# Kernel tuning notes

Measured on AMD Instinct MI355X. Metric: run time of the kernel, lower is better.

The kernel has to match this reference:

```python
import jax, jax.numpy as jnp
import numpy as np

B, S, H, HK, D = 2, 2048, 32, 8, 128
R = 128            # rotary_dim
SINK = 128         # sink_len (always-visible prefix tokens in KV cache)
MAXPOS = 4096
BASE = 10000.0
SCALE = 0.08838834764831845  # 1/sqrt(head_size)
NEG = -1e30


def setup_inputs() -> dict:
    key = jax.random.key(0)
    ks = jax.random.split(key, 5)
    q = jax.random.normal(ks[0], (B, S, H, D), jnp.float32)
    k = jax.random.normal(ks[1], (B, S, HK, D), jnp.float32)
    v = jax.random.normal(ks[2], (B, S, HK, D), jnp.float32)
    sink_k = jax.random.normal(ks[3], (B, SINK, HK, D), jnp.float32)
    sink_v = jax.random.normal(ks[4], (B, SINK, HK, D), jnp.float32)
    # vLLM-style cache: row p = concat(cos(p*inv_freq), sin(p*inv_freq)), each R/2 wide
    inv_freq = 1.0 / (BASE ** (jnp.arange(0, R, 2, dtype=jnp.float32) / R))
    t = jnp.arange(MAXPOS, dtype=jnp.float32)
    freqs = jnp.outer(t, inv_freq)                      # [MAXPOS, R/2]
    cos_sin_cache = jnp.concatenate([jnp.cos(freqs), jnp.sin(freqs)], axis=-1)
    positions = jnp.arange(S, dtype=jnp.int32)
    return {"q": q, "k": k, "v": v, "sink_k": sink_k, "sink_v": sink_v,
            "cos_sin_cache": cos_sin_cache, "positions": positions}


def _apply_rope_neox(x, cos, sin):
    # x: [B, S, N, D]; cos/sin: [S, R/2]
    x_rot, x_pass = x[..., :R], x[..., R:]
    half = R // 2
    x1, x2 = x_rot[..., :half], x_rot[..., half:]
    c = cos[None, :, None, :]
    s = sin[None, :, None, :]
    o1 = x1 * c - x2 * s
    o2 = x2 * c + x1 * s
    return jnp.concatenate([o1, o2, x_pass], axis=-1)


def reference(q, k, v, sink_k, sink_v, cos_sin_cache, positions):
    # RoPE on q and k (sink KV already cached post-RoPE at their positions)
    cos_sin = cos_sin_cache[positions]                  # [S, R]
    cos, sin = cos_sin[:, :R // 2], cos_sin[:, R // 2:]
    q = _apply_rope_neox(q, cos, sin)
    k = _apply_rope_neox(k, cos, sin)

    # Prepend sink KV: effective kv length = SINK + S
    k_full = jnp.concatenate([sink_k, k], axis=1)       # [B, SINK+S, HK, D]
    v_full = jnp.concatenate([sink_v, v], axis=1)

    # GQA: expand kv heads to query heads
    rep = H // HK
    k_full = jnp.repeat(k_full, rep, axis=2)            # [B, SINK+S, H, D]
    v_full = jnp.repeat(v_full, rep, axis=2)

    scores = jnp.einsum('bqhd,bkhd->bhqk', q, k_full) * SCALE  # [B,H,S,SINK+S]

    # sink tokens always visible; causal over the real sequence
    q_idx = jnp.arange(S)[:, None]
    k_idx = jnp.arange(SINK + S)[None, :]
    mask = (k_idx < SINK) | ((k_idx - SINK) <= q_idx)   # [S, SINK+S]
    scores = jnp.where(mask[None, None], scores, NEG)

    attn = jax.nn.softmax(scores, axis=-1)
    out = jnp.einsum('bhqk,bkhd->bqhd', attn, v_full)   # [B,S,H,D]
    return out
```

## Files before the change

kernel.cpp:

```cpp
#include <hip/hip_runtime.h>

#define B_    2
#define S_    2048
#define H_    32
#define HK_   8
#define D_    128
#define SINK_ 128
#define KV_   (SINK_ + S_)
#define SCALE_L2E 0.12752139f

typedef unsigned short u16;
typedef unsigned int   u32;
typedef float  f32x4  __attribute__((ext_vector_type(4)));
typedef __bf16 bf16x8 __attribute__((ext_vector_type(8)));
typedef short  s16x8  __attribute__((ext_vector_type(8)));

__device__ __forceinline__ u16 f2bf(float f) {
    union { float f; u32 u; } c; c.f = f;
    u32 u = c.u;
    return (u16)((u + 0x7FFFu + ((u >> 16) & 1u)) >> 16);
}

#define PREPK_BLOCKS 8704
#define PREPV_BLOCKS 544

__global__ __launch_bounds__(256) void prep_kv(
    const float* __restrict__ k, const float* __restrict__ sk,
    const float* __restrict__ v, const float* __restrict__ sv,
    const float* __restrict__ csc, const int* __restrict__ pos,
    u16* __restrict__ kall,
    u16* __restrict__ vt)
{
    __shared__ u16 t[128][66];
    const int tid = threadIdx.x;
    if ((int)blockIdx.x < PREPK_BLOCKS) {
        int g  = blockIdx.x * 256 + tid;
        int i  = g & 63;
        int rw = g >> 6;
        int bh = rw / KV_;
        int j  = rw - bh * KV_;
        int hk = bh & (HK_ - 1);
        int b  = bh >> 3;
        float o1, o2;
        if (j < SINK_) {
            size_t src = ((size_t)(b * SINK_ + j) * HK_ + hk) * D_;
            o1 = sk[src + i]; o2 = sk[src + 64 + i];
        } else {
            int sq = j - SINK_;
            size_t src = ((size_t)(b * S_ + sq) * HK_ + hk) * D_;
            float x1 = k[src + i];
            float x2 = k[src + 64 + i];
            int p = pos[sq];
            float c = csc[p * D_ + i], sn = csc[p * D_ + 64 + i];
            o1 = x1 * c - x2 * sn;
            o2 = x2 * c + x1 * sn;
        }
        kall[(size_t)rw * D_ + i]      = f2bf(o1);
        kall[(size_t)rw * D_ + 64 + i] = f2bf(o2);
    } else {
        int blk = blockIdx.x - PREPK_BLOCKS;
        int bh = blk / 34;
        int jt = (blk - bh * 34) * 64;
        int hk = bh & (HK_ - 1), b = bh >> 3;
        int d1 = tid & 127;
        int j0 = tid >> 7;
        #pragma unroll
        for (int p = 0; p < 32; ++p) {
            int jl = j0 + 2 * p;
            int j  = jt + jl;
            float x;
            if (j < SINK_) x = sv[((size_t)(b * SINK_ + j) * HK_ + hk) * D_ + d1];
            else           x = v[((size_t)(b * S_ + (j - SINK_)) * HK_ + hk) * D_ + d1];
            t[d1][jl] = f2bf(x);
        }
        __syncthreads();
        int d0 = tid >> 5;
        int jl = (tid & 31) * 2;
        #pragma unroll
        for (int p = 0; p < 16; ++p) {
            int dd = d0 + 8 * p;
            u32 pk = (u32)t[dd][jl] | ((u32)t[dd][jl + 1] << 16);
            *(u32*)(vt + ((size_t)bh * D_ + dd) * KV_ + jt + jl) = pk;
        }
    }
}

__global__ __launch_bounds__(256, 4) void flash_kernel(
    const float* __restrict__ q,
    const float* __restrict__ csc,
    const int*   __restrict__ pos,
    const u16*   __restrict__ kall,
    const u16*   __restrict__ vt,
    float* __restrict__ out)
{
    __shared__ u16 lk[64][136];
    __shared__ u16 lv[128][72];

    const int tid  = threadIdx.x;
    const int lane = tid & 63, w = tid >> 6;
    const int col  = lane & 15, grp = lane >> 4;
    const int rowb = grp * 4;

    const int hk = blockIdx.x & 7;
    int tdec = blockIdx.x >> 3;
    const int b  = tdec & 1; tdec >>= 1;
    const int hr = tdec & 3; tdec >>= 2;
    const int ts = 31 - tdec;
    const int h  = hk * 4 + hr;
    const int s0 = ts * 64;
    const int nfull = 2 + ts;

    const int srow = s0 + w * 16 + col;
    const float* qg = q + ((size_t)(b * S_ + srow) * H_ + h) * D_;
    const float* cp = csc + (size_t)pos[srow] * D_;
    bf16x8 qf[4];
    {
        float xa[4][8], cs0[8], cs1[8], sn0[8], sn1[8];
        #pragma unroll
        for (int c = 0; c < 4; ++c) {
            *(float4*)&xa[c][0] = *(const float4*)(qg + c * 32 + grp * 8);
            *(float4*)&xa[c][4] = *(const float4*)(qg + c * 32 + grp * 8 + 4);
        }
        *(float4*)&cs0[0] = *(const float4*)(cp + grp * 8);
        *(float4*)&cs0[4] = *(const float4*)(cp + grp * 8 + 4);
        *(float4*)&cs1[0] = *(const float4*)(cp + 32 + grp * 8);
        *(float4*)&cs1[4] = *(const float4*)(cp + 32 + grp * 8 + 4);
        *(float4*)&sn0[0] = *(const float4*)(cp + 64 + grp * 8);
        *(float4*)&sn0[4] = *(const float4*)(cp + 64 + grp * 8 + 4);
        *(float4*)&sn1[0] = *(const float4*)(cp + 96 + grp * 8);
        *(float4*)&sn1[4] = *(const float4*)(cp + 96 + grp * 8 + 4);
        #pragma unroll
        for (int j = 0; j < 8; ++j) {
            qf[0][j] = (__bf16)((xa[0][j] * cs0[j] - xa[2][j] * sn0[j]) * SCALE_L2E);
            qf[1][j] = (__bf16)((xa[1][j] * cs1[j] - xa[3][j] * sn1[j]) * SCALE_L2E);
            qf[2][j] = (__bf16)((xa[2][j] * cs0[j] + xa[0][j] * sn0[j]) * SCALE_L2E);
            qf[3][j] = (__bf16)((xa[3][j] * cs1[j] + xa[1][j] * sn1[j]) * SCALE_L2E);
        }
    }

    const u16* kb = kall + (size_t)(b * HK_ + hk) * KV_ * D_;
    const u16* vb = vt   + (size_t)(b * HK_ + hk) * D_ * KV_;

    f32x4 of[8];
    #pragma unroll
    for (int nt = 0; nt < 8; ++nt) of[nt] = (f32x4){0.f, 0.f, 0.f, 0.f};
    float rs = 0.f;

    s16x8 kr[4], vr[4];
    {
        const u16* gk = kb;
        #pragma unroll
        for (int i = 0; i < 4; ++i) {
            int g = tid + i * 256;
            kr[i] = *(const s16x8*)(gk + g * 8);
            vr[i] = *(const s16x8*)(vb + (size_t)(g >> 3) * KV_ + (g & 7) * 8);
        }
    }

    for (int it = 0; it <= nfull; ++it) {
        __syncthreads();
        #pragma unroll
        for (int i = 0; i < 4; ++i) {
            int g = tid + i * 256;
            int j = g >> 4;
            int pj = (j & 0x23) | ((j & 4) << 2) | ((j & 0x18) >> 1);
            *(s16x8*)(&lk[pj][(g & 15) * 8]) = kr[i];
            *(s16x8*)(&lv[g >> 3][(g & 7) * 8]) = vr[i];
        }
        if (it < nfull) {
            const int kt = (it + 1) * 64;
            const u16* gk = kb + (size_t)kt * D_;
            #pragma unroll
            for (int i = 0; i < 4; ++i) {
                int g = tid + i * 256;
                kr[i] = *(const s16x8*)(gk + g * 8);
                vr[i] = *(const s16x8*)(vb + (size_t)(g >> 3) * KV_ + kt + (g & 7) * 8);
            }
        }
        __syncthreads();

        f32x4 sv4[4];
        #pragma unroll
        for (int ct = 0; ct < 4; ++ct) {
            f32x4 acc = (f32x4){0.f, 0.f, 0.f, 0.f};
            #pragma unroll
            for (int c = 0; c < 4; ++c) {
                bf16x8 kf = __builtin_bit_cast(bf16x8,
                    *(const s16x8*)(&lk[ct * 16 + col][c * 32 + grp * 8]));
                acc = __builtin_amdgcn_mfma_f32_16x16x32_bf16(kf, qf[c], acc, 0, 0, 0);
            }
            sv4[ct] = acc;
        }

        if (it == nfull) {
            #pragma unroll
            for (int ct = 0; ct < 4; ++ct) {
                const int keybase = (ct >> 1) * 32 + (ct & 1) * 4 + grp * 8;
                #pragma unroll
                for (int r = 0; r < 4; ++r)
                    if (keybase + r > w * 16 + col) sv4[ct][r] = -1e30f;
            }
        }

        bf16x8 ap[2];
        #pragma unroll
        for (int kc = 0; kc < 2; ++kc) {
            #pragma unroll
            for (int h2 = 0; h2 < 2; ++h2) {
                const int ct = kc * 2 + h2;
                #pragma unroll
                for (int r = 0; r < 4; ++r) {
                    float p = __builtin_amdgcn_exp2f(sv4[ct][r]);
                    __bf16 pb = (__bf16)p;
                    rs += (float)pb;
                    ap[kc][h2 * 4 + r] = pb;
                }
            }
        }

        #pragma unroll
        for (int kc = 0; kc < 2; ++kc) {
            #pragma unroll
            for (int nt = 0; nt < 8; ++nt) {
                bf16x8 bv = __builtin_bit_cast(bf16x8,
                    *(const s16x8*)(&lv[nt * 16 + col][kc * 32 + grp * 8]));
                of[nt] = __builtin_amdgcn_mfma_f32_16x16x32_bf16(ap[kc], bv, of[nt], 0, 0, 0);
            }
        }
    }

    rs += __shfl_xor(rs, 16);
    rs += __shfl_xor(rs, 32);
    float rc[4];
    #pragma unroll
    for (int r = 0; r < 4; ++r)
        rc[r] = 1.0f / __shfl(rs, grp * 4 + r);

    #pragma unroll
    for (int nt = 0; nt < 8; ++nt) {
        #pragma unroll
        for (int r = 0; r < 4; ++r) {
            int sr = s0 + w * 16 + rowb + r;
            out[((size_t)(b * S_ + sr) * H_ + h) * D_ + nt * 16 + col] = of[nt][r] * rc[r];
        }
    }
}

__global__ __launch_bounds__(256) void sink_attn_scalar(
    const float* __restrict__ q, const float* __restrict__ k,
    const float* __restrict__ v, const float* __restrict__ sink_k,
    const float* __restrict__ sink_v, const float* __restrict__ cs_cache,
    const int* __restrict__ positions, float* __restrict__ out)
{
    const int wave = threadIdx.x >> 6;
    const int lane = threadIdx.x & 63;
    const int half = lane >> 5;
    const int l = lane & 31;
    const int d0 = 2 * l;
    const int g = blockIdx.x * 4 + wave;
    const int s = g & (S_ - 1);
    const int bh = g >> 11;
    const int h = bh & (H_ - 1);
    const int b = bh >> 5;
    const int hk = h >> 2;
    const float* cs = cs_cache + positions[s] * D_;
    float2 cq = *(const float2*)(cs + d0);
    float2 sq = *(const float2*)(cs + 64 + d0);
    const float* qrow = q + (size_t)((b * S_ + s) * H_ + h) * D_;
    float2 qa = *(const float2*)(qrow + d0);
    float2 qb = *(const float2*)(qrow + 64 + d0);
    const float q0 = (qa.x * cq.x - qb.x * sq.x) * SCALE_L2E;
    const float q1 = (qa.y * cq.y - qb.y * sq.y) * SCALE_L2E;
    const float q2 = (qb.x * cq.x + qa.x * sq.x) * SCALE_L2E;
    const float q3 = (qb.y * cq.y + qa.y * sq.y) * SCALE_L2E;
    float m = -1e30f, L = 0.0f;
    float a0 = 0.f, a1 = 0.f, a2 = 0.f, a3 = 0.f;
    const int nk = SINK_ + s + 1;
    for (int jj = 0; jj < nk; jj += 2) {
        const int j = jj + half;
        const bool valid = (j < nk);
        const int je = valid ? j : (nk - 1);
        const float* vrow;
        float k0, k1, k2, k3;
        if (je < SINK_) {
            const int off = ((b * SINK_ + je) * HK_ + hk) * D_;
            vrow = sink_v + off;
            float2 ka = *(const float2*)(sink_k + off + d0);
            float2 kb = *(const float2*)(sink_k + off + 64 + d0);
            k0 = ka.x; k1 = ka.y; k2 = kb.x; k3 = kb.y;
        } else {
            const int sk = je - SINK_;
            const int off = ((b * S_ + sk) * HK_ + hk) * D_;
            vrow = v + off;
            float2 ka = *(const float2*)(k + off + d0);
            float2 kb = *(const float2*)(k + off + 64 + d0);
            const float* csk = cs_cache + positions[sk] * D_;
            float2 cc = *(const float2*)(csk + d0);
            float2 ss = *(const float2*)(csk + 64 + d0);
            k0 = ka.x * cc.x - kb.x * ss.x;
            k1 = ka.y * cc.y - kb.y * ss.y;
            k2 = kb.x * cc.x + ka.x * ss.x;
            k3 = kb.y * cc.y + ka.y * ss.y;
        }
        float p = q0 * k0 + q1 * k1 + q2 * k2 + q3 * k3;
        p += __shfl_xor(p, 16); p += __shfl_xor(p, 8);
        p += __shfl_xor(p, 4);  p += __shfl_xor(p, 2); p += __shfl_xor(p, 1);
        if (!valid) p = -1e30f;
        const float mn = fmaxf(m, p);
        const float corr = __builtin_amdgcn_exp2f(m - mn);
        const float pe = __builtin_amdgcn_exp2f(p - mn);
        float2 va = *(const float2*)(vrow + d0);
        float2 vb = *(const float2*)(vrow + 64 + d0);
        L = L * corr + pe;
        a0 = a0 * corr + pe * va.x; a1 = a1 * corr + pe * va.y;
        a2 = a2 * corr + pe * vb.x; a3 = a3 * corr + pe * vb.y;
        m = mn;
    }
    const float mo = __shfl_xor(m, 32);
    const float Lo = __shfl_xor(L, 32);
    const float b0f = __shfl_xor(a0, 32);
    const float b1f = __shfl_xor(a1, 32);
    const float b2f = __shfl_xor(a2, 32);
    const float b3f = __shfl_xor(a3, 32);
    const float M = fmaxf(m, mo);
    const float c_s = __builtin_amdgcn_exp2f(m - M);
    const float c_o = __builtin_amdgcn_exp2f(mo - M);
    const float r = 1.0f / (L * c_s + Lo * c_o);
    float* orow = out + (size_t)((b * S_ + s) * H_ + h) * D_;
    float2 o2v;
    if (half == 0) { o2v.x = (a0 * c_s + b0f * c_o) * r; o2v.y = (a1 * c_s + b1f * c_o) * r; }
    else           { o2v.x = (a2 * c_s + b2f * c_o) * r; o2v.y = (a3 * c_s + b3f * c_o) * r; }
    *(float2*)(orow + half * 64 + d0) = o2v;
}

extern "C" void kernel_launch(void* const* d_in, const int* in_sizes, int n_in,
                              void* d_out, int out_size, void* d_ws, size_t ws_size,
                              hipStream_t stream) {
    const float* q      = (const float*)d_in[0];
    const float* k      = (const float*)d_in[1];
    const float* v      = (const float*)d_in[2];
    const float* sink_k = (const float*)d_in[3];
    const float* sink_v = (const float*)d_in[4];
    const float* cs     = (const float*)d_in[5];
    const int*   pos    = (const int*)d_in[6];
    float* out          = (float*)d_out;

    const size_t kall_elems = (size_t)B_ * HK_ * KV_ * D_;
    const size_t need = 2 * kall_elems * sizeof(u16);

    if (ws_size < need) {
        const int rows = B_ * H_ * S_;
        sink_attn_scalar<<<dim3(rows / 4), dim3(256), 0, stream>>>(
            q, k, v, sink_k, sink_v, cs, pos, out);
        return;
    }

    u16* kall = (u16*)d_ws;
    u16* vtp  = kall + kall_elems;

    prep_kv<<<dim3(PREPK_BLOCKS + PREPV_BLOCKS), dim3(256), 0, stream>>>(
        k, sink_k, v, sink_v, cs, pos, kall, vtp);
    flash_kernel<<<dim3(2048), dim3(256), 0, stream>>>(q, cs, pos, kall, vtp, out);
}
```

Before: 283.5 us.

## Process two 64-row query tiles per block to reuse each K/V tile

Each block now handles 128 query rows as two 64-row halves that share every K/V tile loaded into shared memory. This halves the global and LDS traffic for K and V and halves the grid to 1024 blocks. Causal masking is handled per half, with the final tile fully masked for the first half. In exchange, register use roughly doubles, so the launch bound drops to 2 blocks per CU, and the first half spends MFMA work on one masked tile.

```diff
diff --git a/kernel.cpp b/kernel.cpp
--- a/kernel.cpp
+++ b/kernel.cpp
@@ -85,7 +85,7 @@
     }
 }
 
-__global__ __launch_bounds__(256, 4) void flash_kernel(
+__global__ __launch_bounds__(256, 2) void flash_kernel(
     const float* __restrict__ q,
     const float* __restrict__ csc,
     const int*   __restrict__ pos,
@@ -100,21 +100,23 @@
     const int lane = tid & 63, w = tid >> 6;
     const int col  = lane & 15, grp = lane >> 4;
     const int rowb = grp * 4;
+    const int qcmp = w * 16 + col;
 
     const int hk = blockIdx.x & 7;
     int tdec = blockIdx.x >> 3;
     const int b  = tdec & 1; tdec >>= 1;
     const int hr = tdec & 3; tdec >>= 2;
-    const int ts = 31 - tdec;
+    const int ts = 15 - tdec;
     const int h  = hk * 4 + hr;
-    const int s0 = ts * 64;
-    const int nfull = 2 + ts;
-
-    const int srow = s0 + w * 16 + col;
-    const float* qg = q + ((size_t)(b * S_ + srow) * H_ + h) * D_;
-    const float* cp = csc + (size_t)pos[srow] * D_;
-    bf16x8 qf[4];
-    {
+    const int s0 = ts * 128;
+    const int NT = 2 * ts + 4;
+
+    bf16x8 qf[2][4];
+    #pragma unroll
+    for (int qh = 0; qh < 2; ++qh) {
+        const int srow = s0 + qh * 64 + w * 16 + col;
+        const float* qg = q + ((size_t)(b * S_ + srow) * H_ + h) * D_;
+        const float* cp = csc + (size_t)pos[srow] * D_;
         float xa[4][8], cs0[8], cs1[8], sn0[8], sn1[8];
         #pragma unroll
         for (int c = 0; c < 4; ++c) {
@@ -131,20 +133,23 @@
         *(float4*)&sn1[4] = *(const float4*)(cp + 96 + grp * 8 + 4);
         #pragma unroll
         for (int j = 0; j < 8; ++j) {
-            qf[0][j] = (__bf16)((xa[0][j] * cs0[j] - xa[2][j] * sn0[j]) * SCALE_L2E);
-            qf[1][j] = (__bf16)((xa[1][j] * cs1[j] - xa[3][j] * sn1[j]) * SCALE_L2E);
-            qf[2][j] = (__bf16)((xa[2][j] * cs0[j] + xa[0][j] * sn0[j]) * SCALE_L2E);
-            qf[3][j] = (__bf16)((xa[3][j] * cs1[j] + xa[1][j] * sn1[j]) * SCALE_L2E);
+            qf[qh][0][j] = (__bf16)((xa[0][j] * cs0[j] - xa[2][j] * sn0[j]) * SCALE_L2E);
+            qf[qh][1][j] = (__bf16)((xa[1][j] * cs1[j] - xa[3][j] * sn1[j]) * SCALE_L2E);
+            qf[qh][2][j] = (__bf16)((xa[2][j] * cs0[j] + xa[0][j] * sn0[j]) * SCALE_L2E);
+            qf[qh][3][j] = (__bf16)((xa[3][j] * cs1[j] + xa[1][j] * sn1[j]) * SCALE_L2E);
         }
     }
 
     const u16* kb = kall + (size_t)(b * HK_ + hk) * KV_ * D_;
     const u16* vb = vt   + (size_t)(b * HK_ + hk) * D_ * KV_;
 
-    f32x4 of[8];
+    f32x4 ofA[8], ofB[8];
     #pragma unroll
-    for (int nt = 0; nt < 8; ++nt) of[nt] = (f32x4){0.f, 0.f, 0.f, 0.f};
-    float rs = 0.f;
+    for (int nt = 0; nt < 8; ++nt) {
+        ofA[nt] = (f32x4){0.f, 0.f, 0.f, 0.f};
+        ofB[nt] = (f32x4){0.f, 0.f, 0.f, 0.f};
+    }
+    float rsA = 0.f, rsB = 0.f;
 
     s16x8 kr[4], vr[4];
     {
@@ -157,7 +162,7 @@
         }
     }
 
-    for (int it = 0; it <= nfull; ++it) {
+    for (int it = 0; it < NT; ++it) {
         __syncthreads();
         #pragma unroll
         for (int i = 0; i < 4; ++i) {
@@ -167,7 +172,7 @@
             *(s16x8*)(&lk[pj][(g & 15) * 8]) = kr[i];
             *(s16x8*)(&lv[g >> 3][(g & 7) * 8]) = vr[i];
         }
-        if (it < nfull) {
+        if (it + 1 < NT) {
             const int kt = (it + 1) * 64;
             const u16* gk = kb + (size_t)kt * D_;
             #pragma unroll
@@ -179,42 +184,37 @@
         }
         __syncthreads();
 
-        f32x4 sv4[4];
+        const bool diagA = (it == NT - 2);
+        const bool lastT = (it == NT - 1);
+
+        bf16x8 apA[2], apB[2];
         #pragma unroll
         for (int ct = 0; ct < 4; ++ct) {
-            f32x4 acc = (f32x4){0.f, 0.f, 0.f, 0.f};
+            f32x4 aA = (f32x4){0.f, 0.f, 0.f, 0.f};
+            f32x4 aB = (f32x4){0.f, 0.f, 0.f, 0.f};
             #pragma unroll
             for (int c = 0; c < 4; ++c) {
                 bf16x8 kf = __builtin_bit_cast(bf16x8,
                     *(const s16x8*)(&lk[ct * 16 + col][c * 32 + grp * 8]));
-                acc = __builtin_amdgcn_mfma_f32_16x16x32_bf16(kf, qf[c], acc, 0, 0, 0);
+                aA = __builtin_amdgcn_mfma_f32_16x16x32_bf16(kf, qf[0][c], aA, 0, 0, 0);
+                aB = __builtin_amdgcn_mfma_f32_16x16x32_bf16(kf, qf[1][c], aB, 0, 0, 0);
             }
-            sv4[ct] = acc;
-        }
-
-        if (it == nfull) {
+            const int keybase = (ct >> 1) * 32 + (ct & 1) * 4 + grp * 8;
             #pragma unroll
-            for (int ct = 0; ct < 4; ++ct) {
-                const int keybase = (ct >> 1) * 32 + (ct & 1) * 4 + grp * 8;
-                #pragma unroll
-                for (int r = 0; r < 4; ++r)
-                    if (keybase + r > w * 16 + col) sv4[ct][r] = -1e30f;
-            }
-        }
-
-        bf16x8 ap[2];
-        #pragma unroll
-        for (int kc = 0; kc < 2; ++kc) {
-            #pragma unroll
-            for (int h2 = 0; h2 < 2; ++h2) {
-                const int ct = kc * 2 + h2;
-                #pragma unroll
-                for (int r = 0; r < 4; ++r) {
-                    float p = __builtin_amdgcn_exp2f(sv4[ct][r]);
-                    __bf16 pb = (__bf16)p;
-                    rs += (float)pb;
-                    ap[kc][h2 * 4 + r] = pb;
-                }
+            for (int r = 0; r < 4; ++r) {
+                const int kap = keybase + r;
+                float sA = aA[r];
+                if ((diagA && kap > qcmp) || lastT) sA = -1e30f;
+                float sB = aB[r];
+                if (lastT && kap > qcmp) sB = -1e30f;
+                float pA = __builtin_amdgcn_exp2f(sA);
+                float pB = __builtin_amdgcn_exp2f(sB);
+                __bf16 bA = (__bf16)pA;
+                __bf16 bB = (__bf16)pB;
+                rsA += (float)bA;
+                rsB += (float)bB;
+                apA[ct >> 1][(ct & 1) * 4 + r] = bA;
+                apB[ct >> 1][(ct & 1) * 4 + r] = bB;
             }
         }
 
@@ -224,24 +224,31 @@
             for (int nt = 0; nt < 8; ++nt) {
                 bf16x8 bv = __builtin_bit_cast(bf16x8,
                     *(const s16x8*)(&lv[nt * 16 + col][kc * 32 + grp * 8]));
-                of[nt] = __builtin_amdgcn_mfma_f32_16x16x32_bf16(ap[kc], bv, of[nt], 0, 0, 0);
+                ofA[nt] = __builtin_amdgcn_mfma_f32_16x16x32_bf16(apA[kc], bv, ofA[nt], 0, 0, 0);
+                ofB[nt] = __builtin_amdgcn_mfma_f32_16x16x32_bf16(apB[kc], bv, ofB[nt], 0, 0, 0);
             }
         }
     }
 
-    rs += __shfl_xor(rs, 16);
-    rs += __shfl_xor(rs, 32);
-    float rc[4];
+    rsA += __shfl_xor(rsA, 16);
+    rsA += __shfl_xor(rsA, 32);
+    rsB += __shfl_xor(rsB, 16);
+    rsB += __shfl_xor(rsB, 32);
+    float rcA[4], rcB[4];
     #pragma unroll
-    for (int r = 0; r < 4; ++r)
-        rc[r] = 1.0f / __shfl(rs, grp * 4 + r);
+    for (int r = 0; r < 4; ++r) {
+        rcA[r] = 1.0f / __shfl(rsA, grp * 4 + r);
+        rcB[r] = 1.0f / __shfl(rsB, grp * 4 + r);
+    }
 
     #pragma unroll
     for (int nt = 0; nt < 8; ++nt) {
         #pragma unroll
         for (int r = 0; r < 4; ++r) {
-            int sr = s0 + w * 16 + rowb + r;
-            out[((size_t)(b * S_ + sr) * H_ + h) * D_ + nt * 16 + col] = of[nt][r] * rc[r];
+            int srA = s0 + w * 16 + rowb + r;
+            out[((size_t)(b * S_ + srA) * H_ + h) * D_ + nt * 16 + col] = ofA[nt][r] * rcA[r];
+            int srB = srA + 64;
+            out[((size_t)(b * S_ + srB) * H_ + h) * D_ + nt * 16 + col] = ofB[nt][r] * rcB[r];
         }
     }
 }
@@ -360,5 +367,5 @@
 
     prep_kv<<<dim3(PREPK_BLOCKS + PREPV_BLOCKS), dim3(256), 0, stream>>>(
         k, sink_k, v, sink_v, cs, pos, kall, vtp);
-    flash_kernel<<<dim3(2048), dim3(256), 0, stream>>>(q, cs, pos, kall, vtp, out);
-}
+    flash_kernel<<<dim3(1024), dim3(256), 0, stream>>>(q, cs, pos, kall, vtp, out);
+}
```

Result: faster. 233.1 us (-17.8%).
